# Kernel optimization log

Measured on AMD Instinct MI355X. Metric: run time of the kernel, lower is better.

Reference implementation:

```python
import jax, jax.numpy as jnp
import numpy as np

B, N, D, H, F = 8, 1024, 1024, 16, 4096
HEAD_DIM = D // H


def layernorm(x, g, b, eps=1e-5):
    m = jnp.mean(x, axis=-1, keepdims=True)
    v = jnp.mean(jnp.square(x - m), axis=-1, keepdims=True)
    return (x - m) * jax.lax.rsqrt(v + eps) * g + b


def setup_inputs() -> dict:
    key = jax.random.key(0)
    ks = jax.random.split(key, 12)
    s = 0.02
    return {
        "src": jax.random.normal(ks[0], (B, N, D), dtype=jnp.float32),
        "mask": jax.random.bernoulli(ks[1], 0.9, (B, N)),  # bool, True = keep token
        "Wqkv": jax.random.normal(ks[2], (3 * D, D), dtype=jnp.float32) * s,
        "Wproj": jax.random.normal(ks[3], (D, D), dtype=jnp.float32) * s,
        "bproj": jnp.zeros((D,), jnp.float32),
        "W1": jax.random.normal(ks[4], (F, D), dtype=jnp.float32) * s,
        "b1": jnp.zeros((F,), jnp.float32),
        "W2": jax.random.normal(ks[5], (D, F), dtype=jnp.float32) * s,
        "b2": jnp.zeros((D,), jnp.float32),
        "g0": jnp.ones((D,), jnp.float32),
        "beta0": jnp.zeros((D,), jnp.float32),
        "g1": jnp.ones((D,), jnp.float32),
        "beta1": jnp.zeros((D,), jnp.float32),
    }


def reference(src, mask, Wqkv, Wproj, bproj, W1, b1, W2, b2, g0, beta0, g1, beta1):
    Bx, Nx, C = src.shape
    # pre-norm + masked self-attention (eval mode: dropouts/drop_path are identity)
    h = layernorm(src, g0, beta0)
    qkv = (h @ Wqkv.T).reshape(Bx, Nx, 3, H, HEAD_DIM).transpose(2, 0, 3, 1, 4)
    q, k, v = qkv[0], qkv[1], qkv[2]  # (B, H, N, head_dim)
    scale = HEAD_DIM ** -0.5
    attn = jnp.einsum('bhnd,bhmd->bhnm', q, k) * scale  # (B, H, N, N)
    pair_mask = (mask[:, None, :] & mask[:, :, None])[:, None, :, :]  # (B,1,N,N)
    neg = -jnp.finfo(attn.dtype).max
    attn = jnp.where(pair_mask, attn, neg)
    attn = jax.nn.softmax(attn, axis=-1)
    a = jnp.einsum('bhnm,bhmd->bhnd', attn, v).transpose(0, 2, 1, 3).reshape(Bx, Nx, C)
    a = a @ Wproj.T + bproj
    x = src + a
    # norm1 + GELU FFN
    x = layernorm(x, g1, beta1)
    ffn = jax.nn.gelu(x @ W1.T + b1, approximate=False) @ W2.T + b2
    return x + ffn
```

## Files before the change

### kernel.cpp

```cpp
#include <hip/hip_runtime.h>
#include <math.h>
#include <stdint.h>
#include <float.h>

#define DEV __device__ __forceinline__

typedef __attribute__((ext_vector_type(8))) short bf16x8;
typedef __attribute__((ext_vector_type(4))) float f32x4;
typedef unsigned short u16;
typedef unsigned int u32;

constexpr int cB = 8, cN = 1024, cD = 1024, cH = 16, cF = 4096, cHD = 64;
constexpr int BH = cB * cH;
constexpr int TOK = cB * cN;

DEV u16 f2bf(float f) {
  u32 x = __float_as_uint(f);
  u32 r = (x + 0x7fffu + ((x >> 16) & 1u)) >> 16;
  return (u16)r;
}

DEV float bf2f(u16 s) { return __uint_as_float(((u32)s) << 16); }

DEV void gl_lds16(const u16* g, u16* l) {
  __builtin_amdgcn_global_load_lds((const __attribute__((address_space(1))) u32*)g,
                                   (__attribute__((address_space(3))) u32*)l, 16, 0, 0);
}

__global__ void mask_norm(const unsigned char* __restrict__ rawb, int* __restrict__ keep) {
  const u32* rawi = (const u32*)rawb;
  const float* rawf = (const float*)rawb;
  int t = threadIdx.x;
  int fb = 0, ff = 0;
  for (int i = t; i < 2048; i += 1024) {
    u32 wv = rawi[i];
    if (wv == 0x3f800000u) ff = 1;
    else if (wv > 1u) fb = 1;
  }
  __shared__ int sf[2];
  if (t == 0) { sf[0] = 0; sf[1] = 0; }
  __syncthreads();
  if (fb) atomicOr(&sf[0], 1);
  if (ff) atomicOr(&sf[1], 1);
  __syncthreads();
  const int isf32 = sf[1];
  const int isbool = sf[0] && !isf32;
  for (int i = t; i < TOK; i += 1024)
    keep[i] = isf32 ? (rawf[i] != 0.f) : (isbool ? (rawb[i] != 0) : (rawi[i] != 0u));
}

__global__ void cvt_k(const float* __restrict__ in, u16* __restrict__ out, int n4) {
  int i = blockIdx.x * blockDim.x + threadIdx.x;
  if (i >= n4) return;
  float4 v = ((const float4*)in)[i];
  short4 o;
  o.x = (short)f2bf(v.x); o.y = (short)f2bf(v.y);
  o.z = (short)f2bf(v.z); o.w = (short)f2bf(v.w);
  ((short4*)out)[i] = o;
}

template <int WF32>
__global__ __launch_bounds__(256) void ln_k(const float* __restrict__ in,
                                            const float* __restrict__ g,
                                            const float* __restrict__ be,
                                            u16* __restrict__ outb,
                                            float* __restrict__ outf) {
  const int row = blockIdx.x;
  const int t = threadIdx.x;
  const float4 v = ((const float4*)(in + (size_t)row * cD))[t];
  float s = v.x + v.y + v.z + v.w;
  float s2 = v.x * v.x + v.y * v.y + v.z * v.z + v.w * v.w;
#pragma unroll
  for (int m = 1; m < 64; m <<= 1) {
    s += __shfl_xor(s, m);
    s2 += __shfl_xor(s2, m);
  }
  __shared__ float ls[8];
  const int w = t >> 6;
  if ((t & 63) == 0) { ls[w] = s; ls[4 + w] = s2; }
  __syncthreads();
  s = ls[0] + ls[1] + ls[2] + ls[3];
  s2 = ls[4] + ls[5] + ls[6] + ls[7];
  const float mean = s * (1.f / cD);
  const float var = fmaxf(s2 * (1.f / cD) - mean * mean, 0.f);
  const float inv = rsqrtf(var + 1e-5f);
  const float4 gg = ((const float4*)g)[t];
  const float4 bb = ((const float4*)be)[t];
  const float o0 = (v.x - mean) * inv * gg.x + bb.x;
  const float o1 = (v.y - mean) * inv * gg.y + bb.y;
  const float o2 = (v.z - mean) * inv * gg.z + bb.z;
  const float o3 = (v.w - mean) * inv * gg.w + bb.w;
  short4 ob;
  ob.x = (short)f2bf(o0); ob.y = (short)f2bf(o1);
  ob.z = (short)f2bf(o2); ob.w = (short)f2bf(o3);
  ((short4*)(outb + (size_t)row * cD))[t] = ob;
  if (WF32) {
    float4 of; of.x = o0; of.y = o1; of.z = o2; of.w = o3;
    ((float4*)(outf + (size_t)row * cD))[t] = of;
  }
}

template <int EP, int BN>
__global__ __launch_bounds__(256) void gemm_bt(const u16* __restrict__ A,
                                               const u16* __restrict__ Bw,
                                               int M, int N, int K, int nbx,
                                               const float* __restrict__ bias,
                                               const float* __restrict__ resid,
                                               float* __restrict__ outf,
                                               u16* __restrict__ ob0,
                                               u16* __restrict__ ob1,
                                               u16* __restrict__ ob2) {
  constexpr int NF = BN / 32;
  __shared__ u16 As[128 * 32];
  __shared__ u16 Bs[BN * 32];
  const int t = threadIdx.x;
  const int l = t & 63;
  const int w = t >> 6;
  const int wr = w >> 1, wc = w & 1;
  const int nwg = gridDim.x;
  const int wgid = (blockIdx.x & 7) * (nwg >> 3) + (blockIdx.x >> 3);
  const int bx = wgid % nbx, by = wgid / nbx;
  const int row0 = by * 128;
  const int col0 = bx * BN;

  f32x4 acc[4][NF] = {};

  const u16* Ag = A + (size_t)(row0 + (t >> 2)) * K + (t & 3) * 8;
  const u16* Bg = Bw + (size_t)(col0 + (t >> 2)) * K + (t & 3) * 8;
  const size_t step64 = (size_t)64 * K;
  u16* ldsA0 = As + (size_t)w * 512;
  u16* ldsA1 = As + 2048 + (size_t)w * 512;
  u16* ldsB0 = Bs + (size_t)w * 512;

  const int fr = l & 15, fk = (l >> 4) * 8;

  for (int k0 = 0; k0 < K; k0 += 32) {
    gl_lds16(Ag + k0, ldsA0);
    gl_lds16(Ag + step64 + k0, ldsA1);
    gl_lds16(Bg + k0, ldsB0);
    if constexpr (BN == 128) {
      u16* ldsB1 = Bs + 2048 + (size_t)w * 512;
      gl_lds16(Bg + step64 + k0, ldsB1);
    }
    __syncthreads();
    bf16x8 af[4], bf[NF];
#pragma unroll
    for (int m = 0; m < 4; ++m)
      af[m] = *(const bf16x8*)&As[(wr * 64 + m * 16 + fr) * 32 + fk];
#pragma unroll
    for (int n = 0; n < NF; ++n)
      bf[n] = *(const bf16x8*)&Bs[(wc * (BN / 2) + n * 16 + fr) * 32 + fk];
#pragma unroll
    for (int m = 0; m < 4; ++m)
#pragma unroll
      for (int n = 0; n < NF; ++n)
        acc[m][n] = __builtin_amdgcn_mfma_f32_16x16x32_bf16(af[m], bf[n], acc[m][n], 0, 0, 0);
    __syncthreads();
  }

#pragma unroll
  for (int m = 0; m < 4; ++m) {
    const int grb = row0 + wr * 64 + m * 16 + (l >> 4) * 4;
#pragma unroll
    for (int n = 0; n < NF; ++n) {
      const int gc = col0 + wc * (BN / 2) + n * 16 + fr;
#pragma unroll
      for (int r = 0; r < 4; ++r) {
        const int gr = grb + r;
        const float cv = acc[m][n][r];
        if constexpr (EP == 0) {
          const int which = gc >> 10;
          const int hh = (gc >> 6) & 15;
          const int dd = gc & 63;
          const int bb = gr >> 10, nn = gr & 1023;
          if (which == 0)
            ob0[(((size_t)bb * cH + hh) * cN + nn) * cHD + dd] = f2bf(cv);
          else if (which == 1)
            ob1[(((size_t)bb * cH + hh) * cN + nn) * cHD + dd] = f2bf(cv);
          else
            ob2[(((size_t)bb * cH + hh) * cHD + dd) * cN + nn] = f2bf(cv);
        } else if constexpr (EP == 1) {
          const size_t idx = (size_t)gr * N + gc;
          outf[idx] = cv + bias[gc] + resid[idx];
        } else if constexpr (EP == 2) {
          const float u = cv + bias[gc];
          const float ge = 0.5f * u * (1.f + erff(u * 0.70710678118654752f));
          ob0[(size_t)gr * N + gc] = f2bf(ge);
        } else {
          const size_t idx = (size_t)gr * N + gc;
          outf[idx] += cv + bias[gc];
        }
      }
    }
  }
}

__global__ __launch_bounds__(256) void attn_k(const u16* __restrict__ Q,
                                              const u16* __restrict__ K,
                                              const u16* __restrict__ Vt,
                                              const int* __restrict__ keep,
                                              u16* __restrict__ out) {
  __shared__ u16 Kbuf[2][32 * 64];
  __shared__ u16 Vbuf[2][64 * 32];
  __shared__ u32 Ps32[4][16 * 20];

  const int t = threadIdx.x, l = t & 63, w = t >> 6;
  const int bh = blockIdx.x, qt = blockIdx.y;
  const int b = bh >> 4, h = bh & 15;
  const u16* Qb = Q + (size_t)bh * cN * cHD;
  const u16* Kb = K + (size_t)bh * cN * cHD;
  const u16* Vb = Vt + (size_t)bh * cHD * cN;
  const int fr = l & 15, fg = l >> 4;
  const int qrow = qt * 64 + w * 16;

  bf16x8 aq0, aq1;
  {
    const bf16x8 q0 = *(const bf16x8*)&Qb[(size_t)(qrow + fr) * cHD + fg * 8];
    const bf16x8 q1 = *(const bf16x8*)&Qb[(size_t)(qrow + fr) * cHD + 32 + fg * 8];
#pragma unroll
    for (int j = 0; j < 8; ++j) {
      aq0[j] = (short)f2bf(bf2f((u16)q0[j]) * 0.125f);
      aq1[j] = (short)f2bf(bf2f((u16)q1[j]) * 0.125f);
    }
  }

  const bool rq = keep[b * cN + qrow + fr] != 0;

  const int p = w * 64 + l;
  const int rK = p >> 3, cK = p & 7;
  const u16* kg = Kb + rK * 64 + ((cK ^ (rK & 7)) * 8);
  const int dV = p >> 2, cV = p & 3;
  const u16* vg = Vb + (size_t)dV * cN + cV * 8;
  u16* ldsK0 = &Kbuf[0][w * 512];
  u16* ldsK1 = &Kbuf[1][w * 512];
  u16* ldsV0 = &Vbuf[0][w * 512];
  u16* ldsV1 = &Vbuf[1][w * 512];

  f32x4 o[4] = {};
  float lpart = 0.f;
  const int kbase = b * cN;
  const int xk0 = (fg ^ (fr & 7)) * 8;
  const int xk1 = ((fg + 4) ^ (fr & 7)) * 8;

  gl_lds16(kg, ldsK0);
  gl_lds16(vg, ldsV0);
  __syncthreads();

  for (int kt = 0; kt < 32; ++kt) {
    const int cur = kt & 1;
    if (kt < 31) {
      gl_lds16(kg + (kt + 1) * 2048, cur ? ldsK0 : ldsK1);
      gl_lds16(vg + (kt + 1) * 32, cur ? ldsV0 : ldsV1);
    }
    const u16* KT = Kbuf[cur];
    const u16* VT = Vbuf[cur];

    float p2[2][4];
#pragma unroll
    for (int n = 0; n < 2; ++n) {
      const int rowoff = (n * 16 + fr) * 64;
      const bf16x8 kA0 = *(const bf16x8*)&KT[rowoff + xk0];
      const bf16x8 kA1 = *(const bf16x8*)&KT[rowoff + xk1];
      f32x4 z = {};
      z = __builtin_amdgcn_mfma_f32_16x16x32_bf16(kA0, aq0, z, 0, 0, 0);
      z = __builtin_amdgcn_mfma_f32_16x16x32_bf16(kA1, aq1, z, 0, 0, 0);
      const int4 kp4 = *(const int4*)&keep[kbase + kt * 32 + n * 16 + fg * 4];
#pragma unroll
      for (int r = 0; r < 4; ++r) {
        const int kpv = (&kp4.x)[r];
        const float pv = rq ? (kpv ? __expf(z[r]) : 0.f) : 1.f;
        p2[n][r] = pv;
        lpart += pv;
      }
    }

#pragma unroll
    for (int n = 0; n < 2; ++n)
#pragma unroll
      for (int rp = 0; rp < 2; ++rp) {
        const u32 dw = (u32)f2bf(p2[n][2 * rp]) | ((u32)f2bf(p2[n][2 * rp + 1]) << 16);
        Ps32[w][fr * 20 + 8 * n + 2 * fg + rp] = dw;
      }
    asm volatile("s_waitcnt lgkmcnt(0)" ::: "memory");
    __builtin_amdgcn_sched_barrier(0);
    const bf16x8 pa = *(const bf16x8*)&Ps32[w][fr * 20 + fg * 4];
#pragma unroll
    for (int n4 = 0; n4 < 4; ++n4) {
      const bf16x8 bv = *(const bf16x8*)&VT[(n4 * 16 + fr) * 32 + fg * 8];
      o[n4] = __builtin_amdgcn_mfma_f32_16x16x32_bf16(pa, bv, o[n4], 0, 0, 0);
    }
    __syncthreads();
  }

  float lsum = lpart;
  lsum += __shfl_xor(lsum, 16);
  lsum += __shfl_xor(lsum, 32);
  float linv[4];
#pragma unroll
  for (int r = 0; r < 4; ++r) linv[r] = 1.f / __shfl(lsum, fg * 4 + r);

#pragma unroll
  for (int n4 = 0; n4 < 4; ++n4) {
#pragma unroll
    for (int r = 0; r < 4; ++r) {
      const int nrow = qrow + fg * 4 + r;
      out[((size_t)b * cN + nrow) * cD + h * 64 + n4 * 16 + fr] = f2bf(o[n4][r] * linv[r]);
    }
  }
}

extern "C" void kernel_launch(void* const* d_in, const int* in_sizes, int n_in,
                              void* d_out, int out_size, void* d_ws, size_t ws_size,
                              hipStream_t stream) {
  (void)in_sizes; (void)n_in; (void)out_size; (void)ws_size;
  const float* src = (const float*)d_in[0];
  const void* maskp = d_in[1];
  const float* Wqkv = (const float*)d_in[2];
  const float* Wproj = (const float*)d_in[3];
  const float* bproj = (const float*)d_in[4];
  const float* W1 = (const float*)d_in[5];
  const float* b1 = (const float*)d_in[6];
  const float* W2 = (const float*)d_in[7];
  const float* b2 = (const float*)d_in[8];
  const float* g0 = (const float*)d_in[9];
  const float* be0 = (const float*)d_in[10];
  const float* g1 = (const float*)d_in[11];
  const float* be1 = (const float*)d_in[12];
  float* out = (float*)d_out;

  char* ws = (char*)d_ws;
  size_t off = 0;
  auto alloc = [&](size_t bytes) -> char* {
    char* p = ws + off;
    off += (bytes + 255) & ~(size_t)255;
    return p;
  };
  u16* wqkv_b = (u16*)alloc((size_t)3 * cD * cD * 2);
  u16* wproj_b = (u16*)alloc((size_t)cD * cD * 2);
  u16* w1_b = (u16*)alloc((size_t)cF * cD * 2);
  u16* w2_b = (u16*)alloc((size_t)cD * cF * 2);
  u16* h_b = (u16*)alloc((size_t)TOK * cD * 2);
  u16* q_b = (u16*)alloc((size_t)TOK * cD * 2);
  u16* k_b = (u16*)alloc((size_t)TOK * cD * 2);
  u16* v_b = (u16*)alloc((size_t)TOK * cD * 2);
  float* x1 = (float*)alloc((size_t)TOK * cD * 4);
  u16* x_b = (u16*)alloc((size_t)TOK * cD * 2);
  u16* f1_b = (u16*)alloc((size_t)TOK * cF * 2);
  int* keep = (int*)alloc((size_t)TOK * 4);

  mask_norm<<<1, 1024, 0, stream>>>((const unsigned char*)maskp, keep);
  cvt_k<<<(3 * cD * cD / 4 + 255) / 256, 256, 0, stream>>>(Wqkv, wqkv_b, 3 * cD * cD / 4);
  cvt_k<<<(cD * cD / 4 + 255) / 256, 256, 0, stream>>>(Wproj, wproj_b, cD * cD / 4);
  cvt_k<<<(cF * cD / 4 + 255) / 256, 256, 0, stream>>>(W1, w1_b, cF * cD / 4);
  cvt_k<<<(cD * cF / 4 + 255) / 256, 256, 0, stream>>>(W2, w2_b, cD * cF / 4);
  ln_k<0><<<TOK, 256, 0, stream>>>(src, g0, be0, h_b, nullptr);

  {
    const int nbx = 3 * cD / 128;
    gemm_bt<0, 128><<<nbx * (TOK / 128), 256, 0, stream>>>(
        h_b, wqkv_b, TOK, 3 * cD, cD, nbx, nullptr, nullptr, nullptr, q_b, k_b, v_b);
  }
  attn_k<<<dim3(BH, cN / 64), 256, 0, stream>>>(q_b, k_b, v_b, keep, h_b);
  {
    const int nbx = cD / 64;
    gemm_bt<1, 64><<<nbx * (TOK / 128), 256, 0, stream>>>(
        h_b, wproj_b, TOK, cD, cD, nbx, bproj, src, x1, nullptr, nullptr, nullptr);
  }
  ln_k<1><<<TOK, 256, 0, stream>>>(x1, g1, be1, x_b, out);
  {
    const int nbx = cF / 128;
    gemm_bt<2, 128><<<nbx * (TOK / 128), 256, 0, stream>>>(
        x_b, w1_b, TOK, cF, cD, nbx, b1, nullptr, nullptr, f1_b, nullptr, nullptr);
  }
  {
    const int nbx = cD / 64;
    gemm_bt<3, 64><<<nbx * (TOK / 128), 256, 0, stream>>>(
        f1_b, w2_b, TOK, cD, cF, nbx, b2, nullptr, out, nullptr, nullptr, nullptr);
  }
}
```

Measured before the change: 614.0 us.

## Double GEMM K-tile to 64 with XOR-swizzled LDS layout

The bf16 GEMM main loop now stages a K=64 slice per iteration instead of K=32. This halves the number of barrier pairs and loop iterations per output tile. The global-to-LDS load mapping is changed to 8 rows by 8 chunks per wave, and the chunk index is XOR-swizzled with the row so fragment reads avoid LDS bank conflicts. It doubles LDS use per block, which may reduce occupancy, and it assumes K is a multiple of 64.

```diff
diff --git a/kernel.cpp b/kernel.cpp
--- a/kernel.cpp
+++ b/kernel.cpp
@@ -111,8 +111,9 @@
                                                u16* __restrict__ ob1,
                                                u16* __restrict__ ob2) {
   constexpr int NF = BN / 32;
-  __shared__ u16 As[128 * 32];
-  __shared__ u16 Bs[BN * 32];
+  constexpr int NBS = BN / 32;
+  __shared__ u16 As[128 * 64];
+  __shared__ u16 Bs[BN * 64];
   const int t = threadIdx.x;
   const int l = t & 63;
   const int w = t >> 6;
@@ -125,36 +126,48 @@
 
   f32x4 acc[4][NF] = {};
 
-  const u16* Ag = A + (size_t)(row0 + (t >> 2)) * K + (t & 3) * 8;
-  const u16* Bg = Bw + (size_t)(col0 + (t >> 2)) * K + (t & 3) * 8;
-  const size_t step64 = (size_t)64 * K;
-  u16* ldsA0 = As + (size_t)w * 512;
-  u16* ldsA1 = As + 2048 + (size_t)w * 512;
-  u16* ldsB0 = Bs + (size_t)w * 512;
-
-  const int fr = l & 15, fk = (l >> 4) * 8;
-
-  for (int k0 = 0; k0 < K; k0 += 32) {
-    gl_lds16(Ag + k0, ldsA0);
-    gl_lds16(Ag + step64 + k0, ldsA1);
-    gl_lds16(Bg + k0, ldsB0);
-    if constexpr (BN == 128) {
-      u16* ldsB1 = Bs + 2048 + (size_t)w * 512;
-      gl_lds16(Bg + step64 + k0, ldsB1);
-    }
+  const int lr = l >> 3, lc = l & 7;
+  const int sc = (lc ^ lr) * 8;
+  const u16* Ag[4];
+  u16* ldsA[4];
+#pragma unroll
+  for (int i = 0; i < 4; ++i) {
+    Ag[i] = A + (size_t)(row0 + i * 32 + w * 8 + lr) * K + sc;
+    ldsA[i] = As + i * 2048 + w * 512;
+  }
+  const u16* Bg[NBS];
+  u16* ldsB[NBS];
+#pragma unroll
+  for (int i = 0; i < NBS; ++i) {
+    Bg[i] = Bw + (size_t)(col0 + i * 32 + w * 8 + lr) * K + sc;
+    ldsB[i] = Bs + i * 2048 + w * 512;
+  }
+
+  const int fr = l & 15, fg = l >> 4;
+  const int fx = fr & 7;
+
+  for (int k0 = 0; k0 < K; k0 += 64) {
+#pragma unroll
+    for (int i = 0; i < 4; ++i) gl_lds16(Ag[i] + k0, ldsA[i]);
+#pragma unroll
+    for (int i = 0; i < NBS; ++i) gl_lds16(Bg[i] + k0, ldsB[i]);
     __syncthreads();
-    bf16x8 af[4], bf[NF];
-#pragma unroll
-    for (int m = 0; m < 4; ++m)
-      af[m] = *(const bf16x8*)&As[(wr * 64 + m * 16 + fr) * 32 + fk];
-#pragma unroll
-    for (int n = 0; n < NF; ++n)
-      bf[n] = *(const bf16x8*)&Bs[(wc * (BN / 2) + n * 16 + fr) * 32 + fk];
-#pragma unroll
-    for (int m = 0; m < 4; ++m)
+#pragma unroll
+    for (int ks = 0; ks < 2; ++ks) {
+      const int xo = ((ks * 4 + fg) ^ fx) * 8;
+      bf16x8 af[4], bfr[NF];
+#pragma unroll
+      for (int m = 0; m < 4; ++m)
+        af[m] = *(const bf16x8*)&As[(wr * 64 + m * 16 + fr) * 64 + xo];
 #pragma unroll
       for (int n = 0; n < NF; ++n)
-        acc[m][n] = __builtin_amdgcn_mfma_f32_16x16x32_bf16(af[m], bf[n], acc[m][n], 0, 0, 0);
+        bfr[n] = *(const bf16x8*)&Bs[(wc * (BN / 2) + n * 16 + fr) * 64 + xo];
+#pragma unroll
+      for (int m = 0; m < 4; ++m)
+#pragma unroll
+        for (int n = 0; n < NF; ++n)
+          acc[m][n] = __builtin_amdgcn_mfma_f32_16x16x32_bf16(af[m], bfr[n], acc[m][n], 0, 0, 0);
+    }
     __syncthreads();
   }
 
```

After: 580.0 us. 5.5% less time.
